# Performance work log

Hardware: AMD Instinct MI355X
Metric: run time of the kernel (lower is better)

The kernel has to match this reference:

```python
import jax, jax.numpy as jnp
import numpy as np

HIDDEN = 256

def setup_inputs() -> dict:
    key = jax.random.key(0)
    ks = jax.random.split(key, 7)
    B, T, L = 64, 128, 32
    H, OUT, IN = HIDDEN, 128, 2
    s = 1.0 / np.sqrt(H)
    return {
        "x": jax.random.normal(ks[0], (B, T, L, IN), dtype=jnp.float32),
        "W_ih": jax.random.uniform(ks[1], (4 * H, IN), jnp.float32, -s, s),
        "W_hh": jax.random.uniform(ks[2], (4 * H, H), jnp.float32, -s, s),
        "b_ih": jax.random.uniform(ks[3], (4 * H,), jnp.float32, -s, s),
        "b_hh": jax.random.uniform(ks[4], (4 * H,), jnp.float32, -s, s),
        "fc_w": jax.random.uniform(ks[5], (128, H), jnp.float32, -s, s),
        "fc_b": jax.random.uniform(ks[6], (128,), jnp.float32, -s, s),
    }

def _lstm_scan(xs, W_ih, W_hh, b_ih, b_hh):
    # xs: [L, N, in]; returns hs: [L, N, H]
    N = xs.shape[1]
    H = W_hh.shape[1]
    h0 = jnp.zeros((N, H), dtype=xs.dtype)
    c0 = jnp.zeros((N, H), dtype=xs.dtype)
    # precompute input projections for all steps: [L, N, 4H]
    x_proj = jnp.einsum('lni,gi->lng', xs, W_ih) + b_ih + b_hh

    def step(carry, xp):
        h, c = carry
        gates = xp + h @ W_hh.T  # [N, 4H]
        i, f, g, o = jnp.split(gates, 4, axis=-1)  # PyTorch gate order i,f,g,o
        c_new = jax.nn.sigmoid(f) * c + jax.nn.sigmoid(i) * jnp.tanh(g)
        h_new = jax.nn.sigmoid(o) * jnp.tanh(c_new)
        return (h_new, c_new), h_new

    _, hs = jax.lax.scan(step, (h0, c0), x_proj)
    return hs

def reference(x, W_ih, W_hh, b_ih, b_hh, fc_w, fc_b):
    B, T, L, IN = x.shape
    xs = x.reshape(B * T, L, IN).transpose(1, 0, 2)  # [L, N, IN], N = B*T
    hs = _lstm_scan(xs, W_ih, W_hh, b_ih, b_hh)      # [L, N, H]
    out = jnp.einsum('lnh,oh->lno', hs, fc_w) + fc_b  # [L, N, OUT]
    out = out.transpose(1, 0, 2).reshape(B, T, L, -1)
    return out
```

## Files before the change

### kernel.cpp

```cpp
#include <hip/hip_runtime.h>

typedef _Float16 f16;
typedef _Float16 f16x8 __attribute__((ext_vector_type(8)));
typedef float f32x4 __attribute__((ext_vector_type(4)));

typedef __attribute__((address_space(1))) const f16 gf16;
typedef __attribute__((address_space(1))) const f16x8 gf16x8;

#define N_TOT   8192
#define L_STEPS 32
#define H_DIM   256
#define OUT_DIM 128
#define BN      32
#define NBLK    256
#define THREADS 512

#define WPACK_OFF  0
#define FCPACK_OFF 524288
#define BSUM_OFF   589824

__global__ __launch_bounds__(256) void prep_kernel(
    const float* __restrict__ W_hh, const float* __restrict__ fc_w,
    const float* __restrict__ b_ih, const float* __restrict__ b_hh,
    f16* __restrict__ Wpack, f16* __restrict__ fcpack, float* __restrict__ bsum)
{
    int p = blockIdx.x * blockDim.x + threadIdx.x;
    if (p < 262144) {
        int e = p & 7, lane = (p >> 3) & 63, T = (p >> 9) & 63, kb = p >> 15;
        int g = 16 * T + (lane & 15);
        int k = 32 * kb + 8 * (lane >> 4) + e;
        Wpack[p] = (f16)W_hh[g * 256 + k];
    } else if (p < 262144 + 32768) {
        int p2 = p - 262144;
        int e = p2 & 7, lane = (p2 >> 3) & 63, ot = (p2 >> 9) & 7, kb = p2 >> 12;
        int o = 16 * ot + (lane & 15);
        int k = 32 * kb + 8 * (lane >> 4) + e;
        fcpack[p2] = (f16)fc_w[o * 256 + k];
    } else if (p < 262144 + 32768 + 1024) {
        int g = p - 262144 - 32768;
        bsum[g] = b_ih[g] + b_hh[g];
    }
}

__device__ __forceinline__ float sigmoid_(float x) {
    return 1.0f / (1.0f + __expf(-x));
}
__device__ __forceinline__ float tanh_(float x) {
    float t = __expf(-2.0f * x);
    return (1.0f - t) / (1.0f + t);
}

__device__ __forceinline__ void lds_barrier() {
    asm volatile("s_waitcnt lgkmcnt(0)" ::: "memory");
    __builtin_amdgcn_s_barrier();
    asm volatile("" ::: "memory");
}

__global__ __launch_bounds__(THREADS, 2) void lstm_kernel(
    const float* __restrict__ x, const float* __restrict__ W_ih,
    const f16* __restrict__ Wpack, const float* __restrict__ bsum,
    const f16* __restrict__ fcpack, const float* __restrict__ fc_b,
    float* __restrict__ out)
{
    __shared__ __align__(16) f16 hp[2][8192];
    __shared__ __align__(16) float obuf[2][BN * OUT_DIM];
    __shared__ __align__(16) float2 xbuf[BN * 34];

    const int tid  = threadIdx.x;
    const int wave = tid >> 6;
    const int lane = tid & 63;
    const int l15  = lane & 15;
    const int lq   = lane >> 4;
    const int n0   = blockIdx.x * BN;
    const int kb0  = (blockIdx.x >> 3) & 7;

    f16x8 fcw[8];
#pragma unroll
    for (int p = 0; p < 8; ++p) {
        int kb = (p + kb0) & 7;
        fcw[p] = *(const f16x8*)&fcpack[((kb * 8 + wave) * 64 + lane) * 8];
    }

    for (int i = tid; i < 8192; i += THREADS) hp[0][i] = (f16)0.0f;

    {
        const int row = tid >> 4, part = tid & 15;
        f32x4 v = *(const f32x4*)&x[(n0 + row) * (L_STEPS * 2) + part * 4];
        xbuf[row * 34 + 2 * part + 0] = make_float2(v[0], v[1]);
        xbuf[row * 34 + 2 * part + 1] = make_float2(v[2], v[3]);
    }

    float wih0[2][4], wih1[2][4], bsv[2][4];
#pragma unroll
    for (int ti = 0; ti < 2; ++ti)
#pragma unroll
        for (int q = 0; q < 4; ++q) {
            int g = 256 * q + 16 * (wave + 8 * ti) + l15;
            wih0[ti][q] = W_ih[g * 2 + 0];
            wih1[ti][q] = W_ih[g * 2 + 1];
            bsv[ti][q]  = bsum[g];
        }
    const float fcbv = fc_b[16 * wave + l15];
    const int   ocol = 16 * wave + l15;

    float c[2][2][4];
#pragma unroll
    for (int ti = 0; ti < 2; ++ti)
#pragma unroll
        for (int mt = 0; mt < 2; ++mt)
#pragma unroll
            for (int r = 0; r < 4; ++r) c[ti][mt][r] = 0.0f;

    unsigned long long wb_u =
        (unsigned long long)(uintptr_t)(Wpack + wave * 512 + lane * 8);

    f16x8 wbuf[2][2][4];
    {
        gf16* wb = (gf16*)(uintptr_t)wb_u;
#pragma unroll
        for (int s = 0; s < 2; ++s) {
            int kb = (kb0 + s) & 7;
#pragma unroll
            for (int ti = 0; ti < 2; ++ti)
#pragma unroll
                for (int q = 0; q < 4; ++q)
                    wbuf[s][ti][q] =
                        *(const gf16x8*)&wb[kb * 32768 + q * 8192 + ti * 4096];
        }
    }

    __syncthreads();

    int buf = 0;
#pragma unroll 1
    for (int l = 0; l < L_STEPS; ++l) {
        const int ob = l & 1;
        asm volatile("" : "+v"(wb_u));
        gf16* wb = (gf16*)(uintptr_t)wb_u;

        float2 xv[2][4];
#pragma unroll
        for (int mt = 0; mt < 2; ++mt)
#pragma unroll
            for (int r = 0; r < 4; ++r)
                xv[mt][r] = xbuf[(16 * mt + 4 * lq + r) * 34 + l];

        f32x4 acc[2][2][4];
#pragma unroll
        for (int mt = 0; mt < 2; ++mt)
#pragma unroll
            for (int r = 0; r < 4; ++r) {
#pragma unroll
                for (int ti = 0; ti < 2; ++ti)
#pragma unroll
                    for (int q = 0; q < 4; ++q)
                        acc[ti][mt][q][r] = bsv[ti][q] + xv[mt][r].x * wih0[ti][q]
                                                       + xv[mt][r].y * wih1[ti][q];
            }

        f32x4 facc0 = {fcbv, fcbv, fcbv, fcbv};
        f32x4 facc1 = facc0;

#pragma unroll
        for (int p = 0; p < 8; ++p) {
            const int s    = p & 1;
            const int kb_c = (p + kb0) & 7;

            f16x8 a0 = *(const f16x8*)&hp[buf][((kb_c * 2 + 0) * 64 + lane) * 8];
            f16x8 a1 = *(const f16x8*)&hp[buf][((kb_c * 2 + 1) * 64 + lane) * 8];
#pragma unroll
            for (int ti = 0; ti < 2; ++ti)
#pragma unroll
                for (int q = 0; q < 4; ++q) {
                    acc[ti][0][q] = __builtin_amdgcn_mfma_f32_16x16x32_f16(
                        a0, wbuf[s][ti][q], acc[ti][0][q], 0, 0, 0);
                    acc[ti][1][q] = __builtin_amdgcn_mfma_f32_16x16x32_f16(
                        a1, wbuf[s][ti][q], acc[ti][1][q], 0, 0, 0);
                }
            facc0 = __builtin_amdgcn_mfma_f32_16x16x32_f16(a0, fcw[p], facc0, 0, 0, 0);
            facc1 = __builtin_amdgcn_mfma_f32_16x16x32_f16(a1, fcw[p], facc1, 0, 0, 0);

            const int kb_n = (p + 2 + kb0) & 7;
#pragma unroll
            for (int ti = 0; ti < 2; ++ti)
#pragma unroll
                for (int q = 0; q < 4; ++q)
                    wbuf[s][ti][q] =
                        *(const gf16x8*)&wb[kb_n * 32768 + q * 8192 + ti * 4096];
        }

#pragma unroll
        for (int r = 0; r < 4; ++r) {
            obuf[ob][(4 * lq + r) * OUT_DIM + ocol]        = facc0[r];
            obuf[ob][(16 + 4 * lq + r) * OUT_DIM + ocol]   = facc1[r];
        }

#pragma unroll
        for (int ti = 0; ti < 2; ++ti) {
            int j   = 16 * (wave + 8 * ti) + l15;
            int kbj = j >> 5, qk = (j >> 3) & 3, e = j & 7;
#pragma unroll
            for (int mt = 0; mt < 2; ++mt)
#pragma unroll
                for (int r = 0; r < 4; ++r) {
                    float gi = acc[ti][mt][0][r];
                    float gf = acc[ti][mt][1][r];
                    float gg = acc[ti][mt][2][r];
                    float go = acc[ti][mt][3][r];
                    float cn = sigmoid_(gf) * c[ti][mt][r] + sigmoid_(gi) * tanh_(gg);
                    c[ti][mt][r] = cn;
                    float hv = sigmoid_(go) * tanh_(cn);
                    int laneA = (4 * lq + r) | (qk << 4);
                    hp[buf ^ 1][((kbj * 2 + mt) * 64 + laneA) * 8 + e] = (f16)hv;
                }
        }
        lds_barrier();

        if (l > 0) {
            const int row = tid >> 4;
            const int gl  = ((n0 + row) * L_STEPS + (l - 1)) * OUT_DIM;
#pragma unroll
            for (int half = 0; half < 2; ++half) {
                int col = (tid & 15) * 4 + half * 64;
                f32x4 v = *(const f32x4*)&obuf[ob][row * OUT_DIM + col];
                *(f32x4*)&out[gl + col] = v;
            }
        }

        buf ^= 1;
    }

    {
        f32x4 e0 = {fcbv, fcbv, fcbv, fcbv};
        f32x4 e1 = e0;
#pragma unroll
        for (int p = 0; p < 8; ++p) {
            const int kb_c = (p + kb0) & 7;
            f16x8 a0 = *(const f16x8*)&hp[buf][((kb_c * 2 + 0) * 64 + lane) * 8];
            f16x8 a1 = *(const f16x8*)&hp[buf][((kb_c * 2 + 1) * 64 + lane) * 8];
            e0 = __builtin_amdgcn_mfma_f32_16x16x32_f16(a0, fcw[p], e0, 0, 0, 0);
            e1 = __builtin_amdgcn_mfma_f32_16x16x32_f16(a1, fcw[p], e1, 0, 0, 0);
        }
#pragma unroll
        for (int r = 0; r < 4; ++r) {
            obuf[0][(4 * lq + r) * OUT_DIM + ocol]        = e0[r];
            obuf[0][(16 + 4 * lq + r) * OUT_DIM + ocol]   = e1[r];
        }
        __syncthreads();
        const int row = tid >> 4;
        const int gl  = ((n0 + row) * L_STEPS + 31) * OUT_DIM;
#pragma unroll
        for (int half = 0; half < 2; ++half) {
            int col = (tid & 15) * 4 + half * 64;
            f32x4 v = *(const f32x4*)&obuf[0][row * OUT_DIM + col];
            *(f32x4*)&out[gl + col] = v;
        }
    }
}

extern "C" void kernel_launch(void* const* d_in, const int* in_sizes, int n_in,
                              void* d_out, int out_size, void* d_ws, size_t ws_size,
                              hipStream_t stream) {
    const float* x    = (const float*)d_in[0];
    const float* W_ih = (const float*)d_in[1];
    const float* W_hh = (const float*)d_in[2];
    const float* b_ih = (const float*)d_in[3];
    const float* b_hh = (const float*)d_in[4];
    const float* fc_w = (const float*)d_in[5];
    const float* fc_b = (const float*)d_in[6];
    float* out = (float*)d_out;

    char* ws = (char*)d_ws;
    f16*   Wpack  = (f16*)(ws + WPACK_OFF);
    f16*   fcpack = (f16*)(ws + FCPACK_OFF);
    float* bsum   = (float*)(ws + BSUM_OFF);

    const int prep_elems = 262144 + 32768 + 1024;
    prep_kernel<<<(prep_elems + 255) / 256, 256, 0, stream>>>(
        W_hh, fc_w, b_ih, b_hh, Wpack, fcpack, bsum);

    lstm_kernel<<<NBLK, THREADS, 0, stream>>>(
        x, W_ih, Wpack, bsum, fcpack, fc_b, out);
}
```

Before: 453.4 us.

## Deepen W_hh prefetch to three stages, stagger per-wave k order, move W_ih to LDS

Adds a third register stage to the W_hh prefetch ring, so each global load has more MFMA work in front of it to hide latency. The per-wave k-block start offset (kb0+wave) staggers the waves so they read different Wpack slices and LDS h-blocks at the same moment. The W_ih and bias values move from registers into shared memory and are reloaded every step, which frees VGPRs to pay for the extra prefetch stage. The cost is more LDS traffic per step and the more complex wraparound prefetch schedule (p%3 with special cases at the end).

Measured after the change: 514.2 us. 1.13x slower.

```diff
diff --git a/kernel.cpp b/kernel.cpp
--- a/kernel.cpp
+++ b/kernel.cpp
@@ -65,6 +65,8 @@
     __shared__ __align__(16) f16 hp[2][8192];
     __shared__ __align__(16) float obuf[2][BN * OUT_DIM];
     __shared__ __align__(16) float2 xbuf[BN * 34];
+    __shared__ __align__(16) float2 cw2[1024];
+    __shared__ float cwb[1024];
 
     const int tid  = threadIdx.x;
     const int wave = tid >> 6;
@@ -73,11 +75,12 @@
     const int lq   = lane >> 4;
     const int n0   = blockIdx.x * BN;
     const int kb0  = (blockIdx.x >> 3) & 7;
+    const int OFF  = (kb0 + wave) & 7;
 
     f16x8 fcw[8];
 #pragma unroll
     for (int p = 0; p < 8; ++p) {
-        int kb = (p + kb0) & 7;
+        int kb = (p + OFF) & 7;
         fcw[p] = *(const f16x8*)&fcpack[((kb * 8 + wave) * 64 + lane) * 8];
     }
 
@@ -89,17 +92,11 @@
         xbuf[row * 34 + 2 * part + 0] = make_float2(v[0], v[1]);
         xbuf[row * 34 + 2 * part + 1] = make_float2(v[2], v[3]);
     }
-
-    float wih0[2][4], wih1[2][4], bsv[2][4];
-#pragma unroll
-    for (int ti = 0; ti < 2; ++ti)
-#pragma unroll
-        for (int q = 0; q < 4; ++q) {
-            int g = 256 * q + 16 * (wave + 8 * ti) + l15;
-            wih0[ti][q] = W_ih[g * 2 + 0];
-            wih1[ti][q] = W_ih[g * 2 + 1];
-            bsv[ti][q]  = bsum[g];
-        }
+    for (int g = tid; g < 1024; g += THREADS) {
+        cw2[g] = make_float2(W_ih[2 * g], W_ih[2 * g + 1]);
+        cwb[g] = bsum[g];
+    }
+
     const float fcbv = fc_b[16 * wave + l15];
     const int   ocol = 16 * wave + l15;
 
@@ -113,13 +110,14 @@
 
     unsigned long long wb_u =
         (unsigned long long)(uintptr_t)(Wpack + wave * 512 + lane * 8);
-
-    f16x8 wbuf[2][2][4];
+    int gbase = 16 * wave + l15;
+
+    f16x8 wbuf[3][2][4];
     {
         gf16* wb = (gf16*)(uintptr_t)wb_u;
 #pragma unroll
-        for (int s = 0; s < 2; ++s) {
-            int kb = (kb0 + s) & 7;
+        for (int s = 0; s < 3; ++s) {
+            int kb = (OFF + s) & 7;
 #pragma unroll
             for (int ti = 0; ti < 2; ++ti)
 #pragma unroll
@@ -137,6 +135,8 @@
         const int ob = l & 1;
         asm volatile("" : "+v"(wb_u));
         gf16* wb = (gf16*)(uintptr_t)wb_u;
+        int gb = gbase;
+        asm volatile("" : "+v"(gb));
 
         float2 xv[2][4];
 #pragma unroll
@@ -147,15 +147,18 @@
 
         f32x4 acc[2][2][4];
 #pragma unroll
-        for (int mt = 0; mt < 2; ++mt)
-#pragma unroll
-            for (int r = 0; r < 4; ++r) {
-#pragma unroll
-                for (int ti = 0; ti < 2; ++ti)
-#pragma unroll
-                    for (int q = 0; q < 4; ++q)
-                        acc[ti][mt][q][r] = bsv[ti][q] + xv[mt][r].x * wih0[ti][q]
-                                                       + xv[mt][r].y * wih1[ti][q];
+        for (int ti = 0; ti < 2; ++ti)
+#pragma unroll
+            for (int q = 0; q < 4; ++q) {
+                int g = 256 * q + 128 * ti + gb;
+                float2 w01 = cw2[g];
+                float  bs  = cwb[g];
+#pragma unroll
+                for (int mt = 0; mt < 2; ++mt)
+#pragma unroll
+                    for (int r = 0; r < 4; ++r)
+                        acc[ti][mt][q][r] = bs + xv[mt][r].x * w01.x
+                                               + xv[mt][r].y * w01.y;
             }
 
         f32x4 facc0 = {fcbv, fcbv, fcbv, fcbv};
@@ -163,8 +166,8 @@
 
 #pragma unroll
         for (int p = 0; p < 8; ++p) {
-            const int s    = p & 1;
-            const int kb_c = (p + kb0) & 7;
+            const int s    = p % 3;
+            const int kb_c = (p + OFF) & 7;
 
             f16x8 a0 = *(const f16x8*)&hp[buf][((kb_c * 2 + 0) * 64 + lane) * 8];
             f16x8 a1 = *(const f16x8*)&hp[buf][((kb_c * 2 + 1) * 64 + lane) * 8];
@@ -180,7 +183,8 @@
             facc0 = __builtin_amdgcn_mfma_f32_16x16x32_f16(a0, fcw[p], facc0, 0, 0, 0);
             facc1 = __builtin_amdgcn_mfma_f32_16x16x32_f16(a1, fcw[p], facc1, 0, 0, 0);
 
-            const int kb_n = (p + 2 + kb0) & 7;
+            const int pn   = (p <= 4) ? (p + 3) : (p == 5 ? 2 : (p == 6 ? 0 : 1));
+            const int kb_n = (pn + OFF) & 7;
 #pragma unroll
             for (int ti = 0; ti < 2; ++ti)
 #pragma unroll
@@ -235,7 +239,7 @@
         f32x4 e1 = e0;
 #pragma unroll
         for (int p = 0; p < 8; ++p) {
-            const int kb_c = (p + kb0) & 7;
+            const int kb_c = (p + OFF) & 7;
             f16x8 a0 = *(const f16x8*)&hp[buf][((kb_c * 2 + 0) * 64 + lane) * 8];
             f16x8 a1 = *(const f16x8*)&hp[buf][((kb_c * 2 + 1) * 64 + lane) * 8];
             e0 = __builtin_amdgcn_mfma_f32_16x16x32_f16(a0, fcw[p], e0, 0, 0, 0);
```

## Triple-buffer W_hh prefetch and compute FC projection after the barrier

Applied to the files above, without the earlier changes.

The W_hh register prefetch becomes a three-stage ring with precomputed byte offsets in place of the two-stage pointer-based scheme, so global loads have more lead time before their MFMAs consume them. The output projection MFMAs move off the recurrent critical path: they run after the step barrier on the freshly written h, overlapping with the next step's wait rather than sitting inside the gate MFMA loop. This shortens the dependency chain per step, at the cost of more VGPRs for the extra weight buffer and a changed obuf indexing and epilogue.

Result: slower. 504.9 us (+11.4%).

```diff
diff --git a/kernel.cpp b/kernel.cpp
--- a/kernel.cpp
+++ b/kernel.cpp
@@ -6,6 +6,7 @@
 
 typedef __attribute__((address_space(1))) const f16 gf16;
 typedef __attribute__((address_space(1))) const f16x8 gf16x8;
+typedef __attribute__((address_space(1))) const char gchar;
 
 #define N_TOT   8192
 #define L_STEPS 32
@@ -76,10 +77,8 @@
 
     f16x8 fcw[8];
 #pragma unroll
-    for (int p = 0; p < 8; ++p) {
-        int kb = (p + kb0) & 7;
-        fcw[p] = *(const f16x8*)&fcpack[((kb * 8 + wave) * 64 + lane) * 8];
-    }
+    for (int kb = 0; kb < 8; ++kb)
+        fcw[kb] = *(const f16x8*)&fcpack[((kb * 8 + wave) * 64 + lane) * 8];
 
     for (int i = tid; i < 8192; i += THREADS) hp[0][i] = (f16)0.0f;
 
@@ -111,22 +110,23 @@
 #pragma unroll
             for (int r = 0; r < 4; ++r) c[ti][mt][r] = 0.0f;
 
-    unsigned long long wb_u =
-        (unsigned long long)(uintptr_t)(Wpack + wave * 512 + lane * 8);
-
-    f16x8 wbuf[2][2][4];
-    {
-        gf16* wb = (gf16*)(uintptr_t)wb_u;
-#pragma unroll
-        for (int s = 0; s < 2; ++s) {
-            int kb = (kb0 + s) & 7;
-#pragma unroll
-            for (int ti = 0; ti < 2; ++ti)
-#pragma unroll
-                for (int q = 0; q < 4; ++q)
-                    wbuf[s][ti][q] =
-                        *(const gf16x8*)&wb[kb * 32768 + q * 8192 + ti * 4096];
-        }
+    gchar* wb0 = (gchar*)(uintptr_t)Wpack;
+    unsigned voffB[2][4];
+#pragma unroll
+    for (int ti = 0; ti < 2; ++ti)
+#pragma unroll
+        for (int q = 0; q < 4; ++q)
+            voffB[ti][q] = 2u * (q * 8192 + ti * 4096 + wave * 512 + lane * 8);
+
+    f16x8 wbuf[3][2][4];
+#pragma unroll
+    for (int s = 0; s < 3; ++s) {
+        gchar* base = wb0 + (((kb0 + s) & 7) * 65536);
+#pragma unroll
+        for (int ti = 0; ti < 2; ++ti)
+#pragma unroll
+            for (int q = 0; q < 4; ++q)
+                wbuf[s][ti][q] = *(const gf16x8*)(base + voffB[ti][q]);
     }
 
     __syncthreads();
@@ -134,9 +134,11 @@
     int buf = 0;
 #pragma unroll 1
     for (int l = 0; l < L_STEPS; ++l) {
-        const int ob = l & 1;
-        asm volatile("" : "+v"(wb_u));
-        gf16* wb = (gf16*)(uintptr_t)wb_u;
+#pragma unroll
+        for (int ti = 0; ti < 2; ++ti)
+#pragma unroll
+            for (int q = 0; q < 4; ++q)
+                asm volatile("" : "+v"(voffB[ti][q]));
 
         float2 xv[2][4];
 #pragma unroll
@@ -158,12 +160,9 @@
                                                        + xv[mt][r].y * wih1[ti][q];
             }
 
-        f32x4 facc0 = {fcbv, fcbv, fcbv, fcbv};
-        f32x4 facc1 = facc0;
-
 #pragma unroll
         for (int p = 0; p < 8; ++p) {
-            const int s    = p & 1;
+            const int s    = p % 3;
             const int kb_c = (p + kb0) & 7;
 
             f16x8 a0 = *(const f16x8*)&hp[buf][((kb_c * 2 + 0) * 64 + lane) * 8];
@@ -177,22 +176,14 @@
                     acc[ti][1][q] = __builtin_amdgcn_mfma_f32_16x16x32_f16(
                         a1, wbuf[s][ti][q], acc[ti][1][q], 0, 0, 0);
                 }
-            facc0 = __builtin_amdgcn_mfma_f32_16x16x32_f16(a0, fcw[p], facc0, 0, 0, 0);
-            facc1 = __builtin_amdgcn_mfma_f32_16x16x32_f16(a1, fcw[p], facc1, 0, 0, 0);
-
-            const int kb_n = (p + 2 + kb0) & 7;
+
+            const int pn   = (p <= 4) ? (p + 3) : (p == 5 ? 2 : (p == 6 ? 0 : 1));
+            gchar* base = wb0 + (((pn + kb0) & 7) * 65536);
 #pragma unroll
             for (int ti = 0; ti < 2; ++ti)
 #pragma unroll
                 for (int q = 0; q < 4; ++q)
-                    wbuf[s][ti][q] =
-                        *(const gf16x8*)&wb[kb_n * 32768 + q * 8192 + ti * 4096];
-        }
-
-#pragma unroll
-        for (int r = 0; r < 4; ++r) {
-            obuf[ob][(4 * lq + r) * OUT_DIM + ocol]        = facc0[r];
-            obuf[ob][(16 + 4 * lq + r) * OUT_DIM + ocol]   = facc1[r];
+                    wbuf[s][ti][q] = *(const gf16x8*)(base + voffB[ti][q]);
         }
 
 #pragma unroll
@@ -222,37 +213,39 @@
 #pragma unroll
             for (int half = 0; half < 2; ++half) {
                 int col = (tid & 15) * 4 + half * 64;
-                f32x4 v = *(const f32x4*)&obuf[ob][row * OUT_DIM + col];
+                f32x4 v = *(const f32x4*)&obuf[(l - 1) & 1][row * OUT_DIM + col];
                 *(f32x4*)&out[gl + col] = v;
             }
         }
 
+        {
+            f32x4 facc0 = {fcbv, fcbv, fcbv, fcbv};
+            f32x4 facc1 = facc0;
+#pragma unroll
+            for (int kb = 0; kb < 8; ++kb) {
+                f16x8 a0 = *(const f16x8*)&hp[buf ^ 1][((kb * 2 + 0) * 64 + lane) * 8];
+                f16x8 a1 = *(const f16x8*)&hp[buf ^ 1][((kb * 2 + 1) * 64 + lane) * 8];
+                facc0 = __builtin_amdgcn_mfma_f32_16x16x32_f16(a0, fcw[kb], facc0, 0, 0, 0);
+                facc1 = __builtin_amdgcn_mfma_f32_16x16x32_f16(a1, fcw[kb], facc1, 0, 0, 0);
+            }
+#pragma unroll
+            for (int r = 0; r < 4; ++r) {
+                obuf[l & 1][(4 * lq + r) * OUT_DIM + ocol]      = facc0[r];
+                obuf[l & 1][(16 + 4 * lq + r) * OUT_DIM + ocol] = facc1[r];
+            }
+        }
+
         buf ^= 1;
     }
 
+    __syncthreads();
     {
-        f32x4 e0 = {fcbv, fcbv, fcbv, fcbv};
-        f32x4 e1 = e0;
-#pragma unroll
-        for (int p = 0; p < 8; ++p) {
-            const int kb_c = (p + kb0) & 7;
-            f16x8 a0 = *(const f16x8*)&hp[buf][((kb_c * 2 + 0) * 64 + lane) * 8];
-            f16x8 a1 = *(const f16x8*)&hp[buf][((kb_c * 2 + 1) * 64 + lane) * 8];
-            e0 = __builtin_amdgcn_mfma_f32_16x16x32_f16(a0, fcw[p], e0, 0, 0, 0);
-            e1 = __builtin_amdgcn_mfma_f32_16x16x32_f16(a1, fcw[p], e1, 0, 0, 0);
-        }
-#pragma unroll
-        for (int r = 0; r < 4; ++r) {
-            obuf[0][(4 * lq + r) * OUT_DIM + ocol]        = e0[r];
-            obuf[0][(16 + 4 * lq + r) * OUT_DIM + ocol]   = e1[r];
-        }
-        __syncthreads();
         const int row = tid >> 4;
         const int gl  = ((n0 + row) * L_STEPS + 31) * OUT_DIM;
 #pragma unroll
         for (int half = 0; half < 2; ++half) {
             int col = (tid & 15) * 4 + half * 64;
-            f32x4 v = *(const f32x4*)&obuf[0][row * OUT_DIM + col];
+            f32x4 v = *(const f32x4*)&obuf[1][row * OUT_DIM + col];
             *(f32x4*)&out[gl + col] = v;
         }
     }
```
